# Kernel tuning notes

Hardware: AMD Instinct MI355X
Metric: run time of the kernel (lower is better)

## Reference

```python
import jax, jax.numpy as jnp
import numpy as np

B, S, H = 64, 512, 768
ATT_H, CLS_H = 100, 300


def setup_inputs() -> dict:
    key = jax.random.key(0)
    ks = jax.random.split(key, 8)
    hidden_states = jax.random.normal(ks[0], (B, S, H), jnp.float32)
    is_cont = jax.random.bernoulli(ks[1], 0.25, (B, S)).at[:, 0].set(False)
    offset_mapping = jnp.stack(
        [is_cont.astype(jnp.int32) * 3, jnp.zeros((B, S), jnp.int32)], axis=-1
    )
    labels = jax.random.randint(ks[2], (B, S), -1, 2).astype(jnp.float32)
    s = 0.02
    W1 = jax.random.normal(ks[3], (H, ATT_H), jnp.float32) * s
    b1 = jnp.zeros((ATT_H,), jnp.float32)
    W2 = jax.random.normal(ks[4], (ATT_H, 1), jnp.float32) * s
    b2 = jnp.zeros((1,), jnp.float32)
    W3 = jax.random.normal(ks[5], (H, CLS_H), jnp.float32) * s
    b3 = jnp.zeros((CLS_H,), jnp.float32)
    W4 = jax.random.normal(ks[6], (CLS_H, 1), jnp.float32) * s
    b4 = jnp.zeros((1,), jnp.float32)
    return dict(hidden_states=hidden_states, offset_mapping=offset_mapping,
                labels=labels, W1=W1, b1=b1, W2=W2, b2=b2, W3=W3, b3=b3,
                W4=W4, b4=b4)


def reference(hidden_states, offset_mapping, labels, W1, b1, W2, b2, W3, b3, W4, b4):
    beta = 1.0            # soft_attention_beta
    w_sent, w_tok, w_reg = 1.0, 1.0, 0.01
    Bn, Sn, _ = hidden_states.shape

    # token attention head: sigmoid(tanh(h W1 + b1) W2 + b2) -> [B, S]
    token_att = jax.nn.sigmoid(jnp.tanh(hidden_states @ W1 + b1) @ W2 + b2)[..., 0]

    # --- subword grouping as a single segment-max ---
    # a continuation token (offset[...,0] != 0) belongs to the segment started
    # by the previous non-continuation token (the word root).
    is_cont = offset_mapping[:, :, 0] != 0          # [B, S]
    start = jnp.logical_not(is_cont)
    start_flat = start.reshape(-1)
    seg_id = jnp.cumsum(start_flat.astype(jnp.int32)) - 1   # [B*S]
    vals = token_att.reshape(-1)
    seg_red = jax.ops.segment_max(vals, seg_id, num_segments=Bn * Sn)  # 'max' subword_method
    # scatter the group reduction back onto the word-root position only
    word_att = jnp.where(start_flat, seg_red[seg_id], vals).reshape(Bn, Sn)

    # mask: labelled (!= -1) AND not a subword continuation
    mask = (jnp.logical_and(labels != -1.0, start)).astype(hidden_states.dtype)
    masked = word_att * mask                          # token_logits

    # soft attention pooling over sequence
    p = jnp.power(masked, beta)
    norm = p / jnp.sum(p, axis=1, keepdims=True)      # [B, S]
    pooled = jnp.einsum('bsh,bs->bh', hidden_states, norm)

    sent = jax.nn.sigmoid(jnp.tanh(pooled @ W3 + b3) @ W4 + b4)  # [B, 1]

    # --- losses (_calculate_loss) ---
    sent_labels = jnp.max(labels, axis=1, keepdims=True)          # [B, 1]
    sentence_loss = jnp.sum((sent - sent_labels) ** 2)
    zero_labels = jnp.where(labels == 1.0, labels, 0.0)
    token_loss = jnp.sum((masked - zero_labels) ** 2)
    ones_mask = jnp.where(masked == 0.0, 1.0, masked)
    reg_a = jnp.sum(jnp.min(ones_mask, axis=1, keepdims=True) ** 2)
    reg_b = jnp.sum((jnp.max(masked, axis=1, keepdims=True) - sent_labels) ** 2)
    loss = w_sent * sentence_loss + w_tok * token_loss + w_reg * (reg_a + reg_b)

    return (loss, sentence_loss, token_loss, reg_a, reg_b,
            hidden_states, masked, sent)
```

## Files before the change

kernel.cpp:

```cpp
#include <hip/hip_runtime.h>
#include <math.h>

#define Bn 64
#define Sn 512
#define Hn 768
#define ATT_H 100
#define CLS_H 300
#define Mtok (Bn*Sn)
#define NP 112
#define NT 7

#define W1T_N (NP*Hn)
#define W3T_N (CLS_H*Hn)
#define POOL_N (Bn*Hn)

#define SROW 72
#define SBUF (16*SROW)
#define SWAVE (2*SBUF)

typedef __attribute__((ext_vector_type(8))) short short8;
typedef __attribute__((ext_vector_type(4))) float floatx4;

__device__ inline float sigf(float x) { return 1.0f / (1.0f + expf(-x)); }

__device__ inline unsigned short f2bf(float x) {
    union { float f; unsigned int u; } v; v.f = x;
    unsigned int r = (v.u + 0x7FFFu + ((v.u >> 16) & 1u)) >> 16;
    return (unsigned short)r;
}

__device__ inline float wred_sum(float v) {
    #pragma unroll
    for (int d = 32; d; d >>= 1) v += __shfl_down(v, d, 64);
    return v;
}
__device__ inline float wred_max(float v) {
    #pragma unroll
    for (int d = 32; d; d >>= 1) v = fmaxf(v, __shfl_down(v, d, 64));
    return v;
}
__device__ inline float wred_min(float v) {
    #pragma unroll
    for (int d = 32; d; d >>= 1) v = fminf(v, __shfl_down(v, d, 64));
    return v;
}

__global__ __launch_bounds__(256) void k0_prep(
    const float* __restrict__ W1, const float* __restrict__ b1,
    const float* __restrict__ W2, const float* __restrict__ W3,
    unsigned short* __restrict__ w1t, float* __restrict__ b1w2,
    float* __restrict__ w3t, float* __restrict__ pooled,
    float* __restrict__ zpart)
{
    int idx = blockIdx.x * 256 + threadIdx.x;
    if (idx < W1T_N) {
        int e = idx & 7;
        int lane = (idx >> 3) & 63;
        int t = idx >> 9;
        int ct = t % 7, kstep = t / 7;
        int n = ct * 16 + (lane & 15);
        int k = kstep * 32 + (lane >> 4) * 8 + e;
        float v = (n < ATT_H) ? W1[(size_t)k * ATT_H + n] : 0.f;
        w1t[idx] = f2bf(v);
    } else if (idx < W1T_N + W3T_N) {
        int i = idx - W1T_N;
        int j = i / Hn, k = i - j * Hn;
        w3t[i] = W3[(size_t)k * CLS_H + j];
    } else if (idx < W1T_N + W3T_N + NP) {
        int j = idx - (W1T_N + W3T_N);
        b1w2[2 * j]     = (j < ATT_H) ? b1[j] : 0.f;
        b1w2[2 * j + 1] = (j < ATT_H) ? W2[j] : 0.f;
    } else if (idx < W1T_N + W3T_N + NP + POOL_N) {
        pooled[idx - (W1T_N + W3T_N + NP)] = 0.f;
    } else if (idx < W1T_N + W3T_N + NP + POOL_N + 5 * Bn) {
        zpart[idx - (W1T_N + W3T_N + NP + POOL_N)] = 0.f;
    }
}

__global__ __launch_bounds__(256, 4) void k1_att(
    const float* __restrict__ h, const unsigned short* __restrict__ w1t,
    const float* __restrict__ b1w2, const float* __restrict__ b2,
    float* __restrict__ out_hidden, float* __restrict__ att)
{
    __shared__ __align__(16) short smem[4 * SWAVE];

    const int tid = threadIdx.x;
    const int wave = tid >> 6, lane = tid & 63;
    const int u = lane & 15, q = lane >> 4;
    const int tl = wave >> 1;
    const int g  = wave & 1;
    const int tok0 = blockIdx.x * 32 + tl * 16;

    const int lr = lane >> 4;
    const int lc = (lane & 15) * 4;

    floatx4 acc[NT];
    #pragma unroll
    for (int ct = 0; ct < NT; ct++) acc[ct] = (floatx4)0.f;

    const short8* __restrict__ w1f = (const short8*)w1t;

    #pragma unroll 2
    for (int ch = 0; ch < 6; ch++) {
        const int kbase = g * 384 + ch * 64;
        short* stage = smem + wave * SWAVE + (ch & 1) * SBUF;

        floatx4 v[4];
        #pragma unroll
        for (int j = 0; j < 4; j++) {
            size_t gidx = (size_t)(tok0 + j * 4 + lr) * Hn + kbase + lc;
            v[j] = *(const floatx4*)(h + gidx);
        }
        #pragma unroll
        for (int j = 0; j < 4; j++) {
            size_t gidx = (size_t)(tok0 + j * 4 + lr) * Hn + kbase + lc;
            *(floatx4*)(out_hidden + gidx) = v[j];
            ushort4 bv;
            bv.x = f2bf(v[j].x); bv.y = f2bf(v[j].y);
            bv.z = f2bf(v[j].z); bv.w = f2bf(v[j].w);
            *(ushort4*)(stage + (j * 4 + lr) * SROW + lc) = bv;
        }
        #pragma unroll
        for (int ks = 0; ks < 2; ks++) {
            short8 a = *(const short8*)(stage + u * SROW + ks * 32 + q * 8);
            const int kstep = g * 12 + ch * 2 + ks;
            #pragma unroll
            for (int ct = 0; ct < NT; ct++) {
                short8 bfr = w1f[(kstep * 7 + ct) * 64 + lane];
                acc[ct] = __builtin_amdgcn_mfma_f32_16x16x32_bf16(a, bfr, acc[ct], 0, 0, 0);
            }
        }
    }

    float* cb = (float*)smem;
    __syncthreads();
    if (g == 1) {
        #pragma unroll
        for (int ct = 0; ct < NT; ct++)
            *(floatx4*)(&cb[(tl * 64 + lane) * 28 + ct * 4]) = acc[ct];
    }
    __syncthreads();
    if (g == 0) {
        #pragma unroll
        for (int ct = 0; ct < NT; ct++) {
            floatx4 o = *(const floatx4*)(&cb[(tl * 64 + lane) * 28 + ct * 4]);
            acc[ct] += o;
        }
        float z[4] = {0.f, 0.f, 0.f, 0.f};
        #pragma unroll
        for (int ct = 0; ct < NT; ct++) {
            float2 bw = *(const float2*)(b1w2 + (ct * 16 + u) * 2);
            #pragma unroll
            for (int r = 0; r < 4; r++)
                z[r] += tanhf(acc[ct][r] + bw.x) * bw.y;
        }
        #pragma unroll
        for (int mask = 1; mask < 16; mask <<= 1) {
            #pragma unroll
            for (int r = 0; r < 4; r++) z[r] += __shfl_xor(z[r], mask, 64);
        }
        if (u == 0) {
            float bb2 = b2[0];
            #pragma unroll
            for (int r = 0; r < 4; r++)
                att[tok0 + q * 4 + r] = sigf(z[r] + bb2);
        }
    }
}

__global__ __launch_bounds__(256) void k2_seg(
    const float* __restrict__ att, const int* __restrict__ offset,
    const float* __restrict__ labels, float* __restrict__ masked_out,
    float* __restrict__ sum_m, float* __restrict__ slab_o,
    float* __restrict__ tl_o, float* __restrict__ mino_o,
    float* __restrict__ maxm_o)
{
    const int b = blockIdx.x, tid = threadIdx.x;
    __shared__ float attl[Sn];
    __shared__ int   startl[Sn];
    __shared__ float rsum[4], rtl[4], rsl[4], rmn[4], rmx[4];

    for (int s = tid; s < Sn; s += 256) {
        attl[s] = att[b * Sn + s];
        startl[s] = (offset[(size_t)(b * Sn + s) * 2] == 0) ? 1 : 0;
    }
    __syncthreads();

    float lsum = 0.f, ltl = 0.f, lslab = -1e30f, lmin = 1e30f, lmax = -1e30f;
    for (int s = tid; s < Sn; s += 256) {
        float lab = labels[b * Sn + s];
        int st = startl[s];
        float m = 0.f;
        if (st && lab != -1.0f) {
            m = attl[s];
            for (int t = s + 1; t < Sn && !startl[t]; t++)
                m = fmaxf(m, attl[t]);
        }
        masked_out[b * Sn + s] = m;
        lsum += m;
        float zl = (lab == 1.0f) ? 1.f : 0.f;
        ltl += (m - zl) * (m - zl);
        lslab = fmaxf(lslab, lab);
        float om = (m == 0.f) ? 1.f : m;
        lmin = fminf(lmin, om);
        lmax = fmaxf(lmax, m);
    }
    int wid = tid >> 6, lane = tid & 63;
    lsum = wred_sum(lsum); ltl = wred_sum(ltl);
    lslab = wred_max(lslab); lmin = wred_min(lmin); lmax = wred_max(lmax);
    if (lane == 0) { rsum[wid]=lsum; rtl[wid]=ltl; rsl[wid]=lslab; rmn[wid]=lmin; rmx[wid]=lmax; }
    __syncthreads();
    if (tid == 0) {
        sum_m[b]  = rsum[0]+rsum[1]+rsum[2]+rsum[3];
        tl_o[b]   = rtl[0]+rtl[1]+rtl[2]+rtl[3];
        slab_o[b] = fmaxf(fmaxf(rsl[0],rsl[1]), fmaxf(rsl[2],rsl[3]));
        mino_o[b] = fminf(fminf(rmn[0],rmn[1]), fminf(rmn[2],rmn[3]));
        maxm_o[b] = fmaxf(fmaxf(rmx[0],rmx[1]), fmaxf(rmx[2],rmx[3]));
    }
}

__global__ __launch_bounds__(192) void k3_pool(
    const float* __restrict__ h, const float* __restrict__ masked,
    const float* __restrict__ sum_m, float* __restrict__ pooled)
{
    const int b = blockIdx.x, sc = blockIdx.y;
    const int tid = threadIdx.x;
    __shared__ float nrm[16];
    if (tid < 16)
        nrm[tid] = masked[b * Sn + sc * 16 + tid] * (1.0f / sum_m[b]);
    __syncthreads();
    const floatx4* hp = (const floatx4*)(h + ((size_t)b * Sn + sc * 16) * Hn) + tid;
    float ax = 0.f, ay = 0.f, az = 0.f, aw = 0.f;
    #pragma unroll 8
    for (int s = 0; s < 16; s++) {
        floatx4 v = hp[(size_t)s * (Hn / 4)];
        float w = nrm[s];
        ax += v.x * w; ay += v.y * w; az += v.z * w; aw += v.w * w;
    }
    float* pp = pooled + (size_t)b * Hn + tid * 4;
    atomicAdd(pp + 0, ax); atomicAdd(pp + 1, ay);
    atomicAdd(pp + 2, az); atomicAdd(pp + 3, aw);
}

__global__ __launch_bounds__(256) void k4_sent(
    const float* __restrict__ pooled, const float* __restrict__ w3t,
    const float* __restrict__ b3, const float* __restrict__ W4,
    float* __restrict__ zpart)
{
    const int b = blockIdx.x, jc = blockIdx.y;
    const int tid = threadIdx.x;
    __shared__ __align__(16) float pl[Hn];
    __shared__ float yred[64];
    for (int k = tid; k < Hn; k += 256) pl[k] = pooled[(size_t)b * Hn + k];
    if (tid < 64) yred[tid] = 0.f;
    __syncthreads();
    int jj = tid >> 2, ks = tid & 3;
    float a = 0.f;
    if (jj < 60) {
        int j = jc * 60 + jj;
        const floatx4* wr = (const floatx4*)(w3t + (size_t)j * Hn) + ks * 48;
        const floatx4* pr = (const floatx4*)pl + ks * 48;
        #pragma unroll 8
        for (int i = 0; i < 48; i++) {
            floatx4 wv = wr[i]; floatx4 pv = pr[i];
            a += wv.x * pv.x + wv.y * pv.y + wv.z * pv.z + wv.w * pv.w;
        }
    }
    a += __shfl_xor(a, 1, 64);
    a += __shfl_xor(a, 2, 64);
    if (jj < 60 && ks == 0) {
        int j = jc * 60 + jj;
        yred[jj] = tanhf(a + b3[j]) * W4[j];
    }
    __syncthreads();
    if (tid < 64) {
        float y = yred[tid];
        y = wred_sum(y);
        if (tid == 0) zpart[jc * Bn + b] = y;
    }
}

__global__ __launch_bounds__(64) void k5_loss(
    const float* __restrict__ zpart, const float* __restrict__ b4,
    const float* __restrict__ slab, const float* __restrict__ tl,
    const float* __restrict__ mino, const float* __restrict__ maxm,
    float* __restrict__ out, float* __restrict__ out_sent)
{
    int t = threadIdx.x;
    float z = b4[0];
    #pragma unroll
    for (int jc = 0; jc < 5; jc++) z += zpart[jc * Bn + t];
    float sent = sigf(z);
    out_sent[t] = sent;
    float sl = slab[t];
    float e1 = (sent - sl) * (sent - sl);
    float e2 = tl[t];
    float e3 = mino[t] * mino[t];
    float mm = maxm[t] - sl;
    float e4 = mm * mm;
    e1 = wred_sum(e1); e2 = wred_sum(e2); e3 = wred_sum(e3); e4 = wred_sum(e4);
    if (t == 0) {
        out[1] = e1;
        out[2] = e2;
        out[3] = e3;
        out[4] = e4;
        out[0] = e1 + e2 + 0.01f * (e3 + e4);
    }
}

extern "C" void kernel_launch(void* const* d_in, const int* in_sizes, int n_in,
                              void* d_out, int out_size, void* d_ws, size_t ws_size,
                              hipStream_t stream) {
    (void)in_sizes; (void)n_in; (void)out_size; (void)ws_size;
    const float* h      = (const float*)d_in[0];
    const int*   offset = (const int*)d_in[1];
    const float* labels = (const float*)d_in[2];
    const float* W1     = (const float*)d_in[3];
    const float* b1     = (const float*)d_in[4];
    const float* W2     = (const float*)d_in[5];
    const float* b2     = (const float*)d_in[6];
    const float* W3     = (const float*)d_in[7];
    const float* b3     = (const float*)d_in[8];
    const float* W4     = (const float*)d_in[9];
    const float* b4     = (const float*)d_in[10];

    float* out        = (float*)d_out;
    float* out_hidden = out + 5;
    float* out_masked = out_hidden + (size_t)Bn * Sn * Hn;
    float* out_sent   = out_masked + (size_t)Bn * Sn;

    float* ws      = (float*)d_ws;
    float* att     = ws;
    float* sum_m   = att + Mtok;
    float* slab    = sum_m + Bn;
    float* tlb     = slab + Bn;
    float* mino    = tlb + Bn;
    float* maxm    = mino + Bn;
    float* pooled  = maxm + Bn;
    float* zpart   = pooled + POOL_N;
    float* b1w2    = zpart + 5 * Bn;
    float* w3t     = b1w2 + 2 * NP;
    unsigned short* w1t = (unsigned short*)(w3t + W3T_N);

    int k0_total = W1T_N + W3T_N + NP + POOL_N + 5 * Bn;
    k0_prep<<<(k0_total + 255) / 256, 256, 0, stream>>>(W1, b1, W2, W3,
                                                        w1t, b1w2, w3t, pooled, zpart);
    k1_att<<<Mtok / 32, 256, 0, stream>>>(h, w1t, b1w2, b2, out_hidden, att);
    k2_seg<<<Bn, 256, 0, stream>>>(att, offset, labels, out_masked,
                                   sum_m, slab, tlb, mino, maxm);
    k3_pool<<<dim3(Bn, 32), 192, 0, stream>>>(h, out_masked, sum_m, pooled);
    k4_sent<<<dim3(Bn, 5), 256, 0, stream>>>(pooled, w3t, b3, W4, zpart);
    k5_loss<<<1, 64, 0, stream>>>(zpart, b4, slab, tlb, mino, maxm, out, out_sent);
}
```

Measured before the change: 302.0 us.

## Restructure attention GEMM: each wave covers 32 tokens over a quarter of K

Measured after the change: 342.6 us. 1.13x slower.

```diff
diff --git a/kernel.cpp b/kernel.cpp
--- a/kernel.cpp
+++ b/kernel.cpp
@@ -13,10 +13,6 @@
 #define W1T_N (NP*Hn)
 #define W3T_N (CLS_H*Hn)
 #define POOL_N (Bn*Hn)
-
-#define SROW 72
-#define SBUF (16*SROW)
-#define SWAVE (2*SBUF)
 
 typedef __attribute__((ext_vector_type(8))) short short8;
 typedef __attribute__((ext_vector_type(4))) float floatx4;
@@ -82,88 +78,108 @@
     const float* __restrict__ b1w2, const float* __restrict__ b2,
     float* __restrict__ out_hidden, float* __restrict__ att)
 {
-    __shared__ __align__(16) short smem[4 * SWAVE];
+    __shared__ __align__(16) char smem[4 * 2 * 32 * 128];
 
     const int tid = threadIdx.x;
     const int wave = tid >> 6, lane = tid & 63;
     const int u = lane & 15, q = lane >> 4;
-    const int tl = wave >> 1;
-    const int g  = wave & 1;
-    const int tok0 = blockIdx.x * 32 + tl * 16;
+    const int g = wave;
+    const int tok0 = blockIdx.x * 32;
 
     const int lr = lane >> 4;
-    const int lc = (lane & 15) * 4;
-
-    floatx4 acc[NT];
-    #pragma unroll
-    for (int ct = 0; ct < NT; ct++) acc[ct] = (floatx4)0.f;
+    const int lcb = (lane & 15) * 8;
+
+    floatx4 acc[2][NT];
+    #pragma unroll
+    for (int mt = 0; mt < 2; mt++)
+        #pragma unroll
+        for (int ct = 0; ct < NT; ct++) acc[mt][ct] = (floatx4)0.f;
 
     const short8* __restrict__ w1f = (const short8*)w1t;
-
-    #pragma unroll 2
-    for (int ch = 0; ch < 6; ch++) {
-        const int kbase = g * 384 + ch * 64;
-        short* stage = smem + wave * SWAVE + (ch & 1) * SBUF;
-
-        floatx4 v[4];
+    char* const sbase = smem + wave * (2 * 32 * 128);
+
+    floatx4 v[8];
+    #pragma unroll
+    for (int j = 0; j < 8; j++) {
+        size_t gidx = (size_t)(tok0 + j * 4 + lr) * Hn + g * 192 + lcb / 2;
+        v[j] = *(const floatx4*)(h + gidx);
+    }
+
+    #pragma unroll
+    for (int ch = 0; ch < 3; ch++) {
+        char* stage = sbase + (ch & 1) * (32 * 128);
+        const int kbase = g * 192 + ch * 64;
+
         #pragma unroll
-        for (int j = 0; j < 4; j++) {
-            size_t gidx = (size_t)(tok0 + j * 4 + lr) * Hn + kbase + lc;
-            v[j] = *(const floatx4*)(h + gidx);
-        }
-        #pragma unroll
-        for (int j = 0; j < 4; j++) {
-            size_t gidx = (size_t)(tok0 + j * 4 + lr) * Hn + kbase + lc;
+        for (int j = 0; j < 8; j++) {
+            int row = j * 4 + lr;
+            size_t gidx = (size_t)(tok0 + row) * Hn + kbase + lcb / 2;
             *(floatx4*)(out_hidden + gidx) = v[j];
             ushort4 bv;
             bv.x = f2bf(v[j].x); bv.y = f2bf(v[j].y);
             bv.z = f2bf(v[j].z); bv.w = f2bf(v[j].w);
-            *(ushort4*)(stage + (j * 4 + lr) * SROW + lc) = bv;
-        }
+            *(ushort4*)(stage + row * 128 + (lcb ^ ((row & 7) << 4))) = bv;
+        }
+
+        if (ch < 2) {
+            #pragma unroll
+            for (int j = 0; j < 8; j++) {
+                size_t gidx = (size_t)(tok0 + j * 4 + lr) * Hn + kbase + 64 + lcb / 2;
+                v[j] = *(const floatx4*)(h + gidx);
+            }
+        }
+
         #pragma unroll
         for (int ks = 0; ks < 2; ks++) {
-            short8 a = *(const short8*)(stage + u * SROW + ks * 32 + q * 8);
-            const int kstep = g * 12 + ch * 2 + ks;
+            const int kstep = g * 6 + ch * 2 + ks;
+            short8 a0 = *(const short8*)(stage + (u) * 128
+                                         + ((ks * 64 + q * 16) ^ ((u & 7) << 4)));
+            short8 a1 = *(const short8*)(stage + (16 + u) * 128
+                                         + ((ks * 64 + q * 16) ^ ((u & 7) << 4)));
             #pragma unroll
             for (int ct = 0; ct < NT; ct++) {
                 short8 bfr = w1f[(kstep * 7 + ct) * 64 + lane];
-                acc[ct] = __builtin_amdgcn_mfma_f32_16x16x32_bf16(a, bfr, acc[ct], 0, 0, 0);
+                acc[0][ct] = __builtin_amdgcn_mfma_f32_16x16x32_bf16(a0, bfr, acc[0][ct], 0, 0, 0);
+                acc[1][ct] = __builtin_amdgcn_mfma_f32_16x16x32_bf16(a1, bfr, acc[1][ct], 0, 0, 0);
             }
         }
     }
 
     float* cb = (float*)smem;
-    __syncthreads();
-    if (g == 1) {
-        #pragma unroll
-        for (int ct = 0; ct < NT; ct++)
-            *(floatx4*)(&cb[(tl * 64 + lane) * 28 + ct * 4]) = acc[ct];
-    }
-    __syncthreads();
-    if (g == 0) {
-        #pragma unroll
-        for (int ct = 0; ct < NT; ct++) {
-            floatx4 o = *(const floatx4*)(&cb[(tl * 64 + lane) * 28 + ct * 4]);
-            acc[ct] += o;
-        }
-        float z[4] = {0.f, 0.f, 0.f, 0.f};
-        #pragma unroll
-        for (int ct = 0; ct < NT; ct++) {
-            float2 bw = *(const float2*)(b1w2 + (ct * 16 + u) * 2);
-            #pragma unroll
-            for (int r = 0; r < 4; r++)
-                z[r] += tanhf(acc[ct][r] + bw.x) * bw.y;
-        }
-        #pragma unroll
-        for (int mask = 1; mask < 16; mask <<= 1) {
-            #pragma unroll
-            for (int r = 0; r < 4; r++) z[r] += __shfl_xor(z[r], mask, 64);
-        }
-        if (u == 0) {
-            float bb2 = b2[0];
-            #pragma unroll
-            for (int r = 0; r < 4; r++)
-                att[tok0 + q * 4 + r] = sigf(z[r] + bb2);
+    #pragma unroll
+    for (int mt = 0; mt < 2; mt++) {
+        __syncthreads();
+        if (g > 0) {
+            #pragma unroll
+            for (int ct = 0; ct < NT; ct++)
+                *(floatx4*)(&cb[((g - 1) * 64 + lane) * 28 + ct * 4]) = acc[mt][ct];
+        }
+        __syncthreads();
+        if (g == 0) {
+            #pragma unroll
+            for (int o = 0; o < 3; o++)
+                #pragma unroll
+                for (int ct = 0; ct < NT; ct++)
+                    acc[mt][ct] += *(const floatx4*)(&cb[(o * 64 + lane) * 28 + ct * 4]);
+            float z[4] = {0.f, 0.f, 0.f, 0.f};
+            #pragma unroll
+            for (int ct = 0; ct < NT; ct++) {
+                float2 bw = *(const float2*)(b1w2 + (ct * 16 + u) * 2);
+                #pragma unroll
+                for (int r = 0; r < 4; r++)
+                    z[r] += tanhf(acc[mt][ct][r] + bw.x) * bw.y;
+            }
+            #pragma unroll
+            for (int mask = 1; mask < 16; mask <<= 1) {
+                #pragma unroll
+                for (int r = 0; r < 4; r++) z[r] += __shfl_xor(z[r], mask, 64);
+            }
+            if (u == 0) {
+                float bb2 = b2[0];
+                #pragma unroll
+                for (int r = 0; r < 4; r++)
+                    att[tok0 + mt * 16 + q * 4 + r] = sigf(z[r] + bb2);
+            }
         }
     }
 }
```
